# Performance work log

Hardware: AMD Instinct MI355X
Metric: run time of the kernel (lower is better)

Reference implementation:

```python
import jax, jax.numpy as jnp
import numpy as np

B, S, E, H = 4, 1024, 1024, 16
HD = E // H  # head_dim = 64
MAX_SEQ = 1024  # rel positions span [-(MAX_SEQ-1), MAX_SEQ-1]


def setup_inputs() -> dict:
    key = jax.random.key(0)
    ks = jax.random.split(key, 12)
    std_e = 1.0 / np.sqrt(E)
    std_h = 1.0 / np.sqrt(HD)
    inp = {
        "x": jax.random.normal(ks[0], (B, S, E), dtype=jnp.float32),
        # torch nn.Linear weights are [out, in]; y = x @ W.T + b
        "Wq": jax.random.uniform(ks[1], (E, E), jnp.float32, -std_e, std_e),
        "bq": jax.random.uniform(ks[2], (E,), jnp.float32, -std_e, std_e),
        "Wk": jax.random.uniform(ks[3], (E, E), jnp.float32, -std_e, std_e),
        "bk": jax.random.uniform(ks[4], (E,), jnp.float32, -std_e, std_e),
        "Wv": jax.random.uniform(ks[5], (E, E), jnp.float32, -std_e, std_e),
        "bv": jax.random.uniform(ks[6], (E,), jnp.float32, -std_e, std_e),
        "Wo": jax.random.uniform(ks[7], (E, E), jnp.float32, -std_e, std_e),
        "bo": jax.random.uniform(ks[8], (E,), jnp.float32, -std_e, std_e),
        # pos_key_proj: Linear(head_dim, head_dim, bias=False)
        "Wp": jax.random.uniform(ks[9], (HD, HD), jnp.float32, -std_h, std_h),
        # learned relative position table [2*max_seq_len-1, head_dim]
        "rel_table": jax.random.normal(ks[10], (2 * MAX_SEQ - 1, HD), dtype=jnp.float32),
    }
    return inp


def _rel_shift(pos_scores):
    # pos_scores: [B, H, S, 2S-1] -> [B, H, S, S]
    # result[..., i, j] = pos_scores[..., i, (S-1) - i + j]
    s = pos_scores.shape[-2]
    idx = (s - 1) - jnp.arange(s)[:, None] + jnp.arange(s)[None, :]  # [S, S]
    return jnp.take_along_axis(pos_scores, idx[None, None, :, :], axis=-1)


def reference(x, Wq, bq, Wk, bk, Wv, bv, Wo, bo, Wp, rel_table):
    scale = 1.0 / np.sqrt(HD)
    Q = (x @ Wq.T + bq).reshape(B, S, H, HD).transpose(0, 2, 1, 3)  # [B,H,S,HD]
    K = (x @ Wk.T + bk).reshape(B, S, H, HD).transpose(0, 2, 1, 3)
    V = (x @ Wv.T + bv).reshape(B, S, H, HD).transpose(0, 2, 1, 3)

    # rel_pos_encoding(S): slice centered at MAX_SEQ-1 covering 2S-1 positions
    center = MAX_SEQ - 1
    rel_emb = rel_table[center - (S - 1): center + S]  # [2S-1, HD]
    rel_key = rel_emb @ Wp.T                            # [2S-1, HD]

    content = jnp.einsum("bhqd,bhkd->bhqk", Q, K) * scale       # [B,H,S,S]
    pos = jnp.einsum("bhqd,pd->bhqp", Q, rel_key) * scale       # [B,H,S,2S-1]
    scores = content + _rel_shift(pos)                          # [B,H,S,S]

    probs = jax.nn.softmax(scores, axis=-1)
    ctx = jnp.einsum("bhqk,bhkd->bhqd", probs, V)               # [B,H,S,HD]
    ctx = ctx.transpose(0, 2, 1, 3).reshape(B, S, E)
    return ctx @ Wo.T + bo
```

## Files before the change

kernel.cpp:

```cpp
#include <hip/hip_runtime.h>
#include <hip/hip_bf16.h>

#define B_   4
#define S_   1024
#define E_   1024
#define H_   16
#define HD_  64

typedef float  f32x4  __attribute__((ext_vector_type(4)));
typedef short  bf16x8 __attribute__((ext_vector_type(8)));
typedef short  bf16x4 __attribute__((ext_vector_type(4)));

__device__ __forceinline__ float bf2f(short u) {
  union { unsigned int i; float f; } v;
  v.i = ((unsigned int)(unsigned short)u) << 16;
  return v.f;
}
__device__ __forceinline__ short f2bf(float f) {
  unsigned int x = __float_as_uint(f);
  x = x + 0x7fffu + ((x >> 16) & 1u);
  return (short)(x >> 16);
}
__device__ __forceinline__ bf16x8 ld_cvt8(const float* __restrict__ p) {
  const f32x4 a = *(const f32x4*)p;
  const f32x4 b = *(const f32x4*)(p + 4);
  bf16x8 r;
  r[0] = f2bf(a[0]); r[1] = f2bf(a[1]); r[2] = f2bf(a[2]); r[3] = f2bf(a[3]);
  r[4] = f2bf(b[0]); r[5] = f2bf(b[1]); r[6] = f2bf(b[2]); r[7] = f2bf(b[3]);
  return r;
}

__device__ __forceinline__ void gload_lds16(const short* g, short* l) {
  __builtin_amdgcn_global_load_lds(
      (const __attribute__((address_space(1))) void*)g,
      (__attribute__((address_space(3))) void*)l, 16, 0, 0);
}

__global__ __launch_bounds__(256) void prep_kernel(
    const float* __restrict__ w0, const float* __restrict__ w1,
    const float* __restrict__ w2, const float* __restrict__ x,
    const float* __restrict__ wo, const float* __restrict__ rel,
    const float* __restrict__ Wp,
    short* __restrict__ WB, short* __restrict__ xbf,
    short* __restrict__ WoB, short* __restrict__ RKw)
{
  const int NW = E_ * E_;
  const int y  = blockIdx.y;

  if (y == 8) {
    if (blockIdx.x >= 32) return;
    const int tid  = threadIdx.x;
    const int lane = tid & 63;
    const int wv   = tid >> 6;
    const int quad = lane >> 4;
    const int l15  = lane & 15;
    const int p0   = blockIdx.x * 64 + wv * 16;

    bf16x8 af[2];
    {
      int prow = p0 + l15; if (prow > 2046) prow = 2046;
      const float* ap = rel + (size_t)prow * 64 + quad * 8;
      af[0] = ld_cvt8(ap);
      af[1] = ld_cvt8(ap + 32);
    }
    f32x4 acc[4] = {};
#pragma unroll
    for (int nt = 0; nt < 4; ++nt) {
      const float* bp = Wp + (size_t)(nt * 16 + l15) * 64 + quad * 8;
      acc[nt] = __builtin_amdgcn_mfma_f32_16x16x32_bf16(af[0], ld_cvt8(bp),      acc[nt], 0, 0, 0);
      acc[nt] = __builtin_amdgcn_mfma_f32_16x16x32_bf16(af[1], ld_cvt8(bp + 32), acc[nt], 0, 0, 0);
    }
#pragma unroll
    for (int r = 0; r < 4; ++r) {
      const int p = p0 + quad * 4 + r;
      if (p < 2047)
#pragma unroll
        for (int nt = 0; nt < 4; ++nt)
          RKw[(size_t)p * 64 + nt * 16 + l15] = f2bf(acc[nt][r]);
    }
    return;
  }

  const float* src;
  short* dst;
  if (y < 3)      { src = (y == 0) ? w0 : (y == 1) ? w1 : w2; dst = WB + (size_t)y * NW; }
  else if (y < 7) { src = x + (size_t)(y - 3) * NW;           dst = xbf + (size_t)(y - 3) * NW; }
  else            { src = wo;                                  dst = WoB; }
  const int i = (blockIdx.x * 256 + threadIdx.x) * 4;
  const f32x4 v = *(const f32x4*)(src + i);
  bf16x4 o;
  o[0] = f2bf(v[0]); o[1] = f2bf(v[1]); o[2] = f2bf(v[2]); o[3] = f2bf(v[3]);
  *(bf16x4*)(dst + i) = o;
}

__global__ __launch_bounds__(256, 3) void gemm_qkv(
    const short* __restrict__ A, const short* __restrict__ W012,
    const float* __restrict__ b0, const float* __restrict__ b1, const float* __restrict__ b2,
    short* __restrict__ Qo, short* __restrict__ Ko, short* __restrict__ Vt)
{
  __shared__ short As[2][128 * 32];
  __shared__ short Bs[2][3 * 64 * 32];

  const int tid  = threadIdx.x;
  const int lane = tid & 63;
  const int wave = tid >> 6;
  const int quad = lane >> 4;
  const int l15  = lane & 15;
  const int wmb  = (wave >> 1) * 64;
  const int wnb  = (wave & 1) * 32;

  const int lid = blockIdx.x;
  const int m0  = ((lid & 7) * 4 + ((lid >> 3) & 3)) * 128;
  const int n0  = (lid >> 5) * 64;

  const int trow = tid >> 2;
  const int tc   = tid & 3;

  auto stage = [&](int k0, int bsel) {
#pragma unroll
    for (int n = 0; n < 2; ++n) {
      const int row  = trow + n * 64;
      const int srcc = tc ^ ((row >> 1) & 3);
      gload_lds16(A + (size_t)(m0 + row) * E_ + k0 + srcc * 8,
                  &As[bsel][n * 2048 + tid * 8]);
    }
    const int srcc = tc ^ ((trow >> 1) & 3);
#pragma unroll
    for (int z = 0; z < 3; ++z)
      gload_lds16(W012 + (size_t)z * E_ * E_ + (size_t)(n0 + trow) * E_ + k0 + srcc * 8,
                  &Bs[bsel][z * 2048 + tid * 8]);
  };

  f32x4 acc[3][4][2] = {};

  stage(0, 0);
  __syncthreads();

#pragma unroll 2
  for (int t = 0; t < 32; ++t) {
    const int cur = t & 1;
    if (t < 31) stage((t + 1) * 32, cur ^ 1);

    bf16x8 af[4];
#pragma unroll
    for (int i = 0; i < 4; ++i) {
      const int row = wmb + i * 16 + l15;
      const int pc  = quad ^ ((row >> 1) & 3);
      af[i] = *(bf16x8*)&As[cur][row * 32 + pc * 8];
    }
#pragma unroll
    for (int z = 0; z < 3; ++z) {
      bf16x8 bfr[2];
#pragma unroll
      for (int j = 0; j < 2; ++j) {
        const int row = wnb + j * 16 + l15;
        const int pc  = quad ^ ((row >> 1) & 3);
        bfr[j] = *(bf16x8*)&Bs[cur][z * 2048 + row * 32 + pc * 8];
      }
#pragma unroll
      for (int i = 0; i < 4; ++i)
#pragma unroll
        for (int j = 0; j < 2; ++j)
          acc[z][i][j] = __builtin_amdgcn_mfma_f32_16x16x32_bf16(af[i], bfr[j], acc[z][i][j], 0, 0, 0);
    }
    __syncthreads();
  }

#pragma unroll
  for (int z = 0; z < 2; ++z) {
    short* C = z ? Ko : Qo;
    const float* bb = z ? b1 : b0;
#pragma unroll
    for (int j = 0; j < 2; ++j) {
      const int n = n0 + wnb + j * 16 + l15;
      const float bv = bb[n];
#pragma unroll
      for (int i = 0; i < 4; ++i) {
        const int m = m0 + wmb + i * 16 + quad * 4;
#pragma unroll
        for (int r = 0; r < 4; ++r)
          C[(size_t)(m + r) * E_ + n] = f2bf(acc[z][i][j][r] + bv);
      }
    }
  }
  {
    const int mtb = m0 + wmb;
    const int bq  = mtb >> 10;
    const int kt  = (mtb >> 6) & 15;
#pragma unroll
    for (int j = 0; j < 2; ++j) {
      const int n = n0 + wnb + j * 16 + l15;
      const float bv = b2[n];
      const int h = (n >> 6) & 15;
      const int d = n & 63;
      bf16x8 lo, hi;
#pragma unroll
      for (int e = 0; e < 8; ++e) {
        lo[e] = f2bf(acc[2][e & 3][j][e >> 2] + bv);
        hi[e] = f2bf(acc[2][e & 3][j][(e >> 2) + 2] + bv);
      }
      const size_t off = ((size_t)((bq * 16 + h) * 64 + d)) * 1024 + kt * 64 + quad * 16;
      *(bf16x8*)(Vt + off)     = lo;
      *(bf16x8*)(Vt + off + 8) = hi;
    }
  }
}

__global__ __launch_bounds__(256) void gemm_out(
    const short* __restrict__ A, const short* __restrict__ W,
    const float* __restrict__ bb, float* __restrict__ C)
{
  __shared__ short As[2][64 * 32];
  __shared__ short Bs[2][128 * 32];

  const int tid  = threadIdx.x;
  const int lane = tid & 63;
  const int wave = tid >> 6;
  const int quad = lane >> 4;
  const int l15  = lane & 15;
  const int wnb  = wave * 32;

  const int lid = blockIdx.x;
  const int m0  = ((lid & 7) * 8 + ((lid >> 3) & 7)) * 64;
  const int n0  = (lid >> 6) * 128;

  const int trow = tid >> 2;
  const int tc   = tid & 3;

  auto stage = [&](int k0, int bsel) {
    {
      const int srcc = tc ^ ((trow >> 1) & 3);
      gload_lds16(A + (size_t)(m0 + trow) * E_ + k0 + srcc * 8, &As[bsel][tid * 8]);
    }
#pragma unroll
    for (int n = 0; n < 2; ++n) {
      const int row  = trow + n * 64;
      const int srcc = tc ^ ((row >> 1) & 3);
      gload_lds16(W + (size_t)(n0 + row) * E_ + k0 + srcc * 8, &Bs[bsel][n * 2048 + tid * 8]);
    }
  };

  f32x4 acc[4][2] = {};

  stage(0, 0);
  __syncthreads();

#pragma unroll 2
  for (int t = 0; t < 32; ++t) {
    const int cur = t & 1;
    if (t < 31) stage((t + 1) * 32, cur ^ 1);

    bf16x8 af[4], bfr[2];
#pragma unroll
    for (int i = 0; i < 4; ++i) {
      const int row = i * 16 + l15;
      const int pc  = quad ^ ((row >> 1) & 3);
      af[i] = *(bf16x8*)&As[cur][row * 32 + pc * 8];
    }
#pragma unroll
    for (int j = 0; j < 2; ++j) {
      const int row = wnb + j * 16 + l15;
      const int pc  = quad ^ ((row >> 1) & 3);
      bfr[j] = *(bf16x8*)&Bs[cur][row * 32 + pc * 8];
    }
#pragma unroll
    for (int i = 0; i < 4; ++i)
#pragma unroll
      for (int j = 0; j < 2; ++j)
        acc[i][j] = __builtin_amdgcn_mfma_f32_16x16x32_bf16(af[i], bfr[j], acc[i][j], 0, 0, 0);
    __syncthreads();
  }

#pragma unroll
  for (int j = 0; j < 2; ++j) {
    const int n = n0 + wnb + j * 16 + l15;
    const float bv = bb[n];
#pragma unroll
    for (int i = 0; i < 4; ++i) {
      const int m = m0 + i * 16 + quad * 4;
#pragma unroll
      for (int r = 0; r < 4; ++r)
        C[(size_t)(m + r) * E_ + n] = acc[i][j][r] + bv;
    }
  }
}

__global__ __launch_bounds__(512, 4) void attn_kernel(
    const short* Qw, const short* __restrict__ Kw,
    const short* __restrict__ Vtg, const short* __restrict__ RKw,
    short* Cw)
{
  __shared__ short Ks[64][72];
  __shared__ short Vt[64][72];
  __shared__ short RKs[256][72];
  __shared__ short Ps[8][16][72];

  const int tid  = threadIdx.x;
  const int lane = tid & 63;
  const int wv   = tid >> 6;
  const int quad = lane >> 4;
  const int l15  = lane & 15;

  const int lid  = blockIdx.x;
  const int pair = (lid & 7) * 8 + (lid >> 6);
  const int qt   = (lid >> 3) & 7;
  const int b    = pair >> 4;
  const int h    = pair & 15;
  const int bh   = pair;
  const int q0   = qt * 128;
  const int qw0  = q0 + wv * 16;
  const int jb   = 112 - 16 * wv;
  const int pbase0 = S_ - 128 - q0;

  bf16x8 qf[2];
  {
    const size_t base = (size_t)(b * S_ + qw0 + l15) * E_ + h * HD_ + quad * 8;
    qf[0] = *(const bf16x8*)(Qw + base);
    qf[1] = *(const bf16x8*)(Qw + base + 32);
  }

  f32x4 oacc[4] = {};
  float lsum[4] = {0.f, 0.f, 0.f, 0.f};

  const float fs = 0.125f * 1.44269504088896340736f;

  const int sr  = tid >> 3;
  const int sc8 = (tid & 7) * 8;

  {
    *(bf16x8*)&Ks[sr][sc8] =
        *(const bf16x8*)(Kw + (size_t)(b * S_ + sr) * E_ + h * HD_ + sc8);
    *(bf16x8*)&Vt[sr][sc8] =
        *(const bf16x8*)(Vtg + (size_t)(bh * 64 + sr) * 1024 + sc8);
#pragma unroll
    for (int jj = 0; jj < 3; ++jj) {
      const int c = tid + jj * 512;
      const int row = c >> 3, ch = (c & 7) * 8;
      int p = pbase0 + row; p = (p > 2046) ? 2046 : p;
      *(bf16x8*)&RKs[row][ch] = *(const bf16x8*)(RKw + (size_t)p * 64 + ch);
    }
    __syncthreads();
  }

#pragma unroll 1
  for (int kt = 0; kt < 16; ++kt) {
    bf16x8 kreg, vreg, rkreg;
    const bool havekv = (kt < 15);
    const bool haverk = (kt < 15);
    if (havekv) {
      kreg = *(const bf16x8*)(Kw + (size_t)(b * S_ + (kt + 1) * 64 + sr) * E_ + h * HD_ + sc8);
      vreg = *(const bf16x8*)(Vtg + (size_t)(bh * 64 + sr) * 1024 + (kt + 1) * 64 + sc8);
    }
    if (haverk) {
      int p = pbase0 + 64 * (kt + 3) + sr; if (p > 2046) p = 2046;
      rkreg = *(const bf16x8*)(RKw + (size_t)p * 64 + sc8);
    }

    f32x4 sc[4] = {};
#pragma unroll
    for (int s = 0; s < 2; ++s) {
#pragma unroll
      for (int kk = 0; kk < 4; ++kk) {
        bf16x8 bf = *(bf16x8*)&Ks[kk*16 + l15][s*32 + quad*8];
        sc[kk] = __builtin_amdgcn_mfma_f32_16x16x32_bf16(qf[s], bf, sc[kk], 0, 0, 0);
      }
    }

    f32x4 ta[5] = {};
#pragma unroll
    for (int jt = 0; jt < 5; ++jt) {
      const int off  = jb + jt * 16;
      const int slot = (kt + (off >> 6)) & 3;
      const int prow = slot * 64 + (off & 63);
#pragma unroll
      for (int s = 0; s < 2; ++s) {
        bf16x8 bf = *(bf16x8*)&RKs[prow + l15][s*32 + quad*8];
        ta[jt] = __builtin_amdgcn_mfma_f32_16x16x32_bf16(qf[s], bf, ta[jt], 0, 0, 0);
      }
    }

    float p[4][4];
#pragma unroll
    for (int r = 0; r < 4; ++r) {
      const int i16 = quad*4 + r;
      const int d   = 15 + l15 - i16;
      const int srcLane = (quad << 4) | (d & 15);
      float sj[5];
#pragma unroll
      for (int jt = 0; jt < 5; ++jt) sj[jt] = __shfl(ta[jt][r], srcLane, 64);
      const bool hi = (d >= 16);
#pragma unroll
      for (int kk = 0; kk < 4; ++kk) {
        const float t = hi ? sj[kk+1] : sj[kk];
        const float sv = fminf((sc[kk][r] + t) * fs, 108.f);
        const float pv = exp2f(sv - 12.f);
        p[kk][r] = pv;
        lsum[r] += pv;
      }
    }

#pragma unroll
    for (int r = 0; r < 4; ++r) {
      bf16x4 pw;
      pw[0] = f2bf(p[0][r]); pw[1] = f2bf(p[1][r]);
      pw[2] = f2bf(p[2][r]); pw[3] = f2bf(p[3][r]);
      *(bf16x4*)&Ps[wv][quad*4 + r][l15*4] = pw;
    }

#pragma unroll
    for (int ks = 0; ks < 2; ++ks) {
      bf16x8 pa = *(bf16x8*)&Ps[wv][l15][ks*32 + quad*8];
#pragma unroll
      for (int dt = 0; dt < 4; ++dt) {
        bf16x8 vb = *(bf16x8*)&Vt[dt*16 + l15][ks*32 + quad*8];
        oacc[dt] = __builtin_amdgcn_mfma_f32_16x16x32_bf16(pa, vb, oacc[dt], 0, 0, 0);
      }
    }

    __syncthreads();
    if (havekv) {
      *(bf16x8*)&Ks[sr][sc8] = kreg;
      *(bf16x8*)&Vt[sr][sc8] = vreg;
    }
    if (haverk) {
      *(bf16x8*)&RKs[((kt + 3) & 3) * 64 + sr][sc8] = rkreg;
    }
    __syncthreads();
  }

#pragma unroll
  for (int off = 1; off <= 8; off <<= 1)
#pragma unroll
    for (int r = 0; r < 4; ++r)
      lsum[r] += __shfl_xor(lsum[r], off, 64);

#pragma unroll
  for (int r = 0; r < 4; ++r) {
    const float inv = 1.0f / lsum[r];
    const size_t row = (size_t)(b * S_ + qw0 + quad*4 + r) * E_ + h * HD_;
#pragma unroll
    for (int dt = 0; dt < 4; ++dt)
      Cw[row + dt*16 + l15] = f2bf(oacc[dt][r] * inv);
  }
}

__global__ void fill_kernel(float* __restrict__ out, int n, float val) {
  for (int i = blockIdx.x * blockDim.x + threadIdx.x; i < n; i += gridDim.x * blockDim.x)
    out[i] = val;
}

extern "C" void kernel_launch(void* const* d_in, const int* in_sizes, int n_in,
                              void* d_out, int out_size, void* d_ws, size_t ws_size,
                              hipStream_t stream)
{
  const size_t WS_NEEDED = 33816448;
  if (ws_size < WS_NEEDED) {
    fill_kernel<<<1024, 256, 0, stream>>>((float*)d_out, out_size, 0.25f);
    return;
  }
  if (n_in != 11 || in_sizes[10] != 2047 * 64) {
    fill_kernel<<<1024, 256, 0, stream>>>((float*)d_out, out_size, 0.75f);
    return;
  }

  const float* x   = (const float*)d_in[0];
  const float* Wq  = (const float*)d_in[1];
  const float* bq  = (const float*)d_in[2];
  const float* Wk  = (const float*)d_in[3];
  const float* bk  = (const float*)d_in[4];
  const float* Wv  = (const float*)d_in[5];
  const float* bv  = (const float*)d_in[6];
  const float* Wo  = (const float*)d_in[7];
  const float* bo  = (const float*)d_in[8];
  const float* Wp  = (const float*)d_in[9];
  const float* rel = (const float*)d_in[10];

  char* ws = (char*)d_ws;
  short* Qws = (short*)(ws);
  short* Kws = (short*)(ws + 8388608);
  short* Vtg = (short*)(ws + 16777216);
  short* WB  = (short*)(ws + 25165824);
  short* WoB = (short*)(ws + 31457280);
  short* RKw = (short*)(ws + 33554432);
  short* xbf = (short*)d_out;

  prep_kernel<<<dim3(1024, 9), dim3(256), 0, stream>>>(
      Wq, Wk, Wv, x, Wo, rel, Wp, WB, xbf, WoB, RKw);

  gemm_qkv<<<dim3(512), dim3(256), 0, stream>>>(
      xbf, WB, bq, bk, bv, Qws, Kws, Vtg);

  attn_kernel<<<dim3(512), dim3(512), 0, stream>>>(Qws, Kws, Vtg, RKw, Qws);

  gemm_out<<<dim3(512), dim3(256), 0, stream>>>(Qws, WoB, bo, (float*)d_out);
}
```

Baseline: 238.5 us.

## Retile QKV and output GEMMs to 128x128 single-buffered tiles

The fused QKV GEMM, which used a 128x64 tile spanning all three weight matrices, becomes a generic 128x128 tile GEMM over the concatenated weights, with 768 blocks that pick Q, K or V output handling from the N offset. The output GEMM moves from 64x128 to 128x128 tiles with 256 blocks. Both kernels drop LDS double buffering in favour of a simple load, sync, compute, sync loop. This raises per-wave MFMA work and operand reuse, but loses the overlap of global loads with compute, and the output GEMM now launches only 256 blocks, which may underfill the GPU.

```diff
diff --git a/kernel.cpp b/kernel.cpp
--- a/kernel.cpp
+++ b/kernel.cpp
@@ -93,13 +93,13 @@
   *(bf16x4*)(dst + i) = o;
 }
 
-__global__ __launch_bounds__(256, 3) void gemm_qkv(
-    const short* __restrict__ A, const short* __restrict__ W012,
+__global__ __launch_bounds__(256) void gemm_cat(
+    const short* __restrict__ A, const short* __restrict__ W,
     const float* __restrict__ b0, const float* __restrict__ b1, const float* __restrict__ b2,
     short* __restrict__ Qo, short* __restrict__ Ko, short* __restrict__ Vt)
 {
-  __shared__ short As[2][128 * 32];
-  __shared__ short Bs[2][3 * 64 * 32];
+  __shared__ short As[128 * 32];
+  __shared__ short Bs[128 * 32];
 
   const int tid  = threadIdx.x;
   const int lane = tid & 63;
@@ -107,177 +107,163 @@
   const int quad = lane >> 4;
   const int l15  = lane & 15;
   const int wmb  = (wave >> 1) * 64;
-  const int wnb  = (wave & 1) * 32;
+  const int wnb  = (wave & 1) * 64;
 
   const int lid = blockIdx.x;
-  const int m0  = ((lid & 7) * 4 + ((lid >> 3) & 3)) * 128;
-  const int n0  = (lid >> 5) * 64;
+  const int idx = lid >> 3;
+  const int m0  = ((lid & 7) * 4 + (idx & 3)) * 128;
+  const int n0  = (idx >> 2) * 128;
 
   const int trow = tid >> 2;
   const int tc   = tid & 3;
 
-  auto stage = [&](int k0, int bsel) {
+  f32x4 acc[4][4] = {};
+
+  for (int k0 = 0; k0 < E_; k0 += 32) {
 #pragma unroll
     for (int n = 0; n < 2; ++n) {
       const int row  = trow + n * 64;
       const int srcc = tc ^ ((row >> 1) & 3);
-      gload_lds16(A + (size_t)(m0 + row) * E_ + k0 + srcc * 8,
-                  &As[bsel][n * 2048 + tid * 8]);
-    }
-    const int srcc = tc ^ ((trow >> 1) & 3);
-#pragma unroll
-    for (int z = 0; z < 3; ++z)
-      gload_lds16(W012 + (size_t)z * E_ * E_ + (size_t)(n0 + trow) * E_ + k0 + srcc * 8,
-                  &Bs[bsel][z * 2048 + tid * 8]);
-  };
-
-  f32x4 acc[3][4][2] = {};
-
-  stage(0, 0);
-  __syncthreads();
-
-#pragma unroll 2
-  for (int t = 0; t < 32; ++t) {
-    const int cur = t & 1;
-    if (t < 31) stage((t + 1) * 32, cur ^ 1);
-
-    bf16x8 af[4];
+      gload_lds16(A + (size_t)(m0 + row) * E_ + k0 + srcc * 8, &As[n * 2048 + tid * 8]);
+    }
+#pragma unroll
+    for (int n = 0; n < 2; ++n) {
+      const int row  = trow + n * 64;
+      const int srcc = tc ^ ((row >> 1) & 3);
+      gload_lds16(W + (size_t)(n0 + row) * E_ + k0 + srcc * 8, &Bs[n * 2048 + tid * 8]);
+    }
+    __syncthreads();
+
+    bf16x8 af[4], bfr[4];
 #pragma unroll
     for (int i = 0; i < 4; ++i) {
       const int row = wmb + i * 16 + l15;
       const int pc  = quad ^ ((row >> 1) & 3);
-      af[i] = *(bf16x8*)&As[cur][row * 32 + pc * 8];
-    }
-#pragma unroll
-    for (int z = 0; z < 3; ++z) {
-      bf16x8 bfr[2];
-#pragma unroll
-      for (int j = 0; j < 2; ++j) {
-        const int row = wnb + j * 16 + l15;
-        const int pc  = quad ^ ((row >> 1) & 3);
-        bfr[j] = *(bf16x8*)&Bs[cur][z * 2048 + row * 32 + pc * 8];
-      }
-#pragma unroll
-      for (int i = 0; i < 4; ++i)
-#pragma unroll
-        for (int j = 0; j < 2; ++j)
-          acc[z][i][j] = __builtin_amdgcn_mfma_f32_16x16x32_bf16(af[i], bfr[j], acc[z][i][j], 0, 0, 0);
-    }
-    __syncthreads();
-  }
-
-#pragma unroll
-  for (int z = 0; z < 2; ++z) {
-    short* C = z ? Ko : Qo;
-    const float* bb = z ? b1 : b0;
-#pragma unroll
-    for (int j = 0; j < 2; ++j) {
-      const int n = n0 + wnb + j * 16 + l15;
-      const float bv = bb[n];
-#pragma unroll
-      for (int i = 0; i < 4; ++i) {
-        const int m = m0 + wmb + i * 16 + quad * 4;
-#pragma unroll
-        for (int r = 0; r < 4; ++r)
-          C[(size_t)(m + r) * E_ + n] = f2bf(acc[z][i][j][r] + bv);
-      }
-    }
-  }
-  {
+      af[i] = *(bf16x8*)&As[row * 32 + pc * 8];
+    }
+#pragma unroll
+    for (int j = 0; j < 4; ++j) {
+      const int row = wnb + j * 16 + l15;
+      const int pc  = quad ^ ((row >> 1) & 3);
+      bfr[j] = *(bf16x8*)&Bs[row * 32 + pc * 8];
+    }
+#pragma unroll
+    for (int i = 0; i < 4; ++i)
+#pragma unroll
+      for (int j = 0; j < 4; ++j)
+        acc[i][j] = __builtin_amdgcn_mfma_f32_16x16x32_bf16(af[i], bfr[j], acc[i][j], 0, 0, 0);
+    __syncthreads();
+  }
+
+  const int z = n0 >> 10;
+  const float* bz = (z == 0) ? b0 : (z == 1) ? b1 : b2;
+
+  if (z == 2) {
     const int mtb = m0 + wmb;
     const int bq  = mtb >> 10;
     const int kt  = (mtb >> 6) & 15;
 #pragma unroll
-    for (int j = 0; j < 2; ++j) {
+    for (int j = 0; j < 4; ++j) {
       const int n = n0 + wnb + j * 16 + l15;
-      const float bv = b2[n];
+      const float bv = bz[n & 1023];
       const int h = (n >> 6) & 15;
       const int d = n & 63;
       bf16x8 lo, hi;
 #pragma unroll
       for (int e = 0; e < 8; ++e) {
-        lo[e] = f2bf(acc[2][e & 3][j][e >> 2] + bv);
-        hi[e] = f2bf(acc[2][e & 3][j][(e >> 2) + 2] + bv);
+        lo[e] = f2bf(acc[e & 3][j][e >> 2] + bv);
+        hi[e] = f2bf(acc[e & 3][j][(e >> 2) + 2] + bv);
       }
       const size_t off = ((size_t)((bq * 16 + h) * 64 + d)) * 1024 + kt * 64 + quad * 16;
       *(bf16x8*)(Vt + off)     = lo;
       *(bf16x8*)(Vt + off + 8) = hi;
     }
-  }
-}
-
-__global__ __launch_bounds__(256) void gemm_out(
+  } else {
+    short* C = z ? Ko : Qo;
+#pragma unroll
+    for (int j = 0; j < 4; ++j) {
+      const int n  = n0 + wnb + j * 16 + l15;
+      const int nc = n & 1023;
+      const float bv = bz[nc];
+#pragma unroll
+      for (int i = 0; i < 4; ++i) {
+        const int m = m0 + wmb + i * 16 + quad * 4;
+#pragma unroll
+        for (int r = 0; r < 4; ++r)
+          C[(size_t)(m + r) * E_ + nc] = f2bf(acc[i][j][r] + bv);
+      }
+    }
+  }
+}
+
+__global__ __launch_bounds__(256) void gemm_o(
     const short* __restrict__ A, const short* __restrict__ W,
     const float* __restrict__ bb, float* __restrict__ C)
 {
-  __shared__ short As[2][64 * 32];
-  __shared__ short Bs[2][128 * 32];
+  __shared__ short As[128 * 32];
+  __shared__ short Bs[128 * 32];
 
   const int tid  = threadIdx.x;
   const int lane = tid & 63;
   const int wave = tid >> 6;
   const int quad = lane >> 4;
   const int l15  = lane & 15;
-  const int wnb  = wave * 32;
+  const int wmb  = (wave >> 1) * 64;
+  const int wnb  = (wave & 1) * 64;
 
   const int lid = blockIdx.x;
-  const int m0  = ((lid & 7) * 8 + ((lid >> 3) & 7)) * 64;
-  const int n0  = (lid >> 6) * 128;
+  const int idx = lid >> 3;
+  const int m0  = ((lid & 7) * 4 + (idx & 3)) * 128;
+  const int n0  = (idx >> 2) * 128;
 
   const int trow = tid >> 2;
   const int tc   = tid & 3;
 
-  auto stage = [&](int k0, int bsel) {
-    {
-      const int srcc = tc ^ ((trow >> 1) & 3);
-      gload_lds16(A + (size_t)(m0 + trow) * E_ + k0 + srcc * 8, &As[bsel][tid * 8]);
-    }
+  f32x4 acc[4][4] = {};
+
+  for (int k0 = 0; k0 < E_; k0 += 32) {
 #pragma unroll
     for (int n = 0; n < 2; ++n) {
       const int row  = trow + n * 64;
       const int srcc = tc ^ ((row >> 1) & 3);
-      gload_lds16(W + (size_t)(n0 + row) * E_ + k0 + srcc * 8, &Bs[bsel][n * 2048 + tid * 8]);
-    }
-  };
-
-  f32x4 acc[4][2] = {};
-
-  stage(0, 0);
-  __syncthreads();
-
-#pragma unroll 2
-  for (int t = 0; t < 32; ++t) {
-    const int cur = t & 1;
-    if (t < 31) stage((t + 1) * 32, cur ^ 1);
-
-    bf16x8 af[4], bfr[2];
+      gload_lds16(A + (size_t)(m0 + row) * E_ + k0 + srcc * 8, &As[n * 2048 + tid * 8]);
+    }
+#pragma unroll
+    for (int n = 0; n < 2; ++n) {
+      const int row  = trow + n * 64;
+      const int srcc = tc ^ ((row >> 1) & 3);
+      gload_lds16(W + (size_t)(n0 + row) * E_ + k0 + srcc * 8, &Bs[n * 2048 + tid * 8]);
+    }
+    __syncthreads();
+
+    bf16x8 af[4], bfr[4];
 #pragma unroll
     for (int i = 0; i < 4; ++i) {
-      const int row = i * 16 + l15;
+      const int row = wmb + i * 16 + l15;
       const int pc  = quad ^ ((row >> 1) & 3);
-      af[i] = *(bf16x8*)&As[cur][row * 32 + pc * 8];
-    }
-#pragma unroll
-    for (int j = 0; j < 2; ++j) {
+      af[i] = *(bf16x8*)&As[row * 32 + pc * 8];
+    }
+#pragma unroll
+    for (int j = 0; j < 4; ++j) {
       const int row = wnb + j * 16 + l15;
       const int pc  = quad ^ ((row >> 1) & 3);
-      bfr[j] = *(bf16x8*)&Bs[cur][row * 32 + pc * 8];
+      bfr[j] = *(bf16x8*)&Bs[row * 32 + pc * 8];
     }
 #pragma unroll
     for (int i = 0; i < 4; ++i)
 #pragma unroll
-      for (int j = 0; j < 2; ++j)
+      for (int j = 0; j < 4; ++j)
         acc[i][j] = __builtin_amdgcn_mfma_f32_16x16x32_bf16(af[i], bfr[j], acc[i][j], 0, 0, 0);
     __syncthreads();
   }
 
 #pragma unroll
-  for (int j = 0; j < 2; ++j) {
+  for (int j = 0; j < 4; ++j) {
     const int n = n0 + wnb + j * 16 + l15;
     const float bv = bb[n];
 #pragma unroll
     for (int i = 0; i < 4; ++i) {
-      const int m = m0 + i * 16 + quad * 4;
+      const int m = m0 + wmb + i * 16 + quad * 4;
 #pragma unroll
       for (int r = 0; r < 4; ++r)
         C[(size_t)(m + r) * E_ + n] = acc[i][j][r] + bv;
@@ -487,10 +473,10 @@
   prep_kernel<<<dim3(1024, 9), dim3(256), 0, stream>>>(
       Wq, Wk, Wv, x, Wo, rel, Wp, WB, xbf, WoB, RKw);
 
-  gemm_qkv<<<dim3(512), dim3(256), 0, stream>>>(
+  gemm_cat<<<dim3(768), dim3(256), 0, stream>>>(
       xbf, WB, bq, bk, bv, Qws, Kws, Vtg);
 
   attn_kernel<<<dim3(512), dim3(512), 0, stream>>>(Qws, Kws, Vtg, RKw, Qws);
 
-  gemm_out<<<dim3(512), dim3(256), 0, stream>>>(Qws, WoB, bo, (float*)d_out);
-}
+  gemm_o<<<dim3(256), dim3(256), 0, stream>>>(Qws, WoB, bo, (float*)d_out);
+}
```

Result: slower. 249.0 us (+4.4%).
